# Kernel tuning notes

Hardware: AMD Instinct MI355X
Metric: run time of the kernel (lower is better)

The kernel has to match this reference:

```python
import jax, jax.numpy as jnp
import numpy as np

B, T, C, H = 1, 4096, 512, 8
HS = C // H  # head size = 64
ROPE_BASE = 10000.0


def setup_inputs() -> dict:
    key = jax.random.key(0)
    k1, k2, k3 = jax.random.split(key, 3)
    x = jax.random.normal(k1, (B, T, C), dtype=jnp.float32)
    W_attn = jax.random.normal(k2, (3 * C, C), dtype=jnp.float32) * 0.02
    W_proj = jax.random.normal(k3, (C, C), dtype=jnp.float32) * 0.02
    # RoPE cache: (T, HS//2, 2) = (cos, sin) per position/frequency
    pos = jnp.arange(T, dtype=jnp.float32)
    inv_freq = 1.0 / (ROPE_BASE ** (jnp.arange(0, HS, 2, dtype=jnp.float32) / HS))
    ang = pos[:, None] * inv_freq[None, :]  # (T, HS//2)
    rope = jnp.stack([jnp.cos(ang), jnp.sin(ang)], axis=-1)
    # causal mask (1,1,T,T), True = attend
    mask = jnp.tril(jnp.ones((T, T), dtype=bool))[None, None]
    return {"x": x, "rope": rope, "mask": mask, "W_attn": W_attn, "W_proj": W_proj}


def apply_rope(x, rope):
    # x: (B, T, H, hs); rope: (>=T, hs//2, 2)
    b, t, h, d = x.shape
    xs = x.reshape(b, t, h, d // 2, 2)
    rc = rope[:t].reshape(1, t, 1, d // 2, 2)
    real = xs[..., 0] * rc[..., 0] - xs[..., 1] * rc[..., 1]
    imag = xs[..., 1] * rc[..., 0] + xs[..., 0] * rc[..., 1]
    return jnp.stack([real, imag], axis=-1).reshape(b, t, h, d)


def reference(x, rope, mask, W_attn, W_proj):
    b, t, c = x.shape
    qkv = x @ W_attn.T  # (B,T,3C)
    q, k, v = jnp.split(qkv, 3, axis=2)
    q = q.reshape(b, t, H, HS)
    k = k.reshape(b, t, H, HS)
    v = v.reshape(b, t, H, HS)
    q = apply_rope(q, rope)
    k = apply_rope(k, rope)
    # (B,H,T,hs)
    q = q.transpose(0, 2, 1, 3)
    k = k.transpose(0, 2, 1, 3)
    v = v.transpose(0, 2, 1, 3)
    scores = jnp.einsum('bhqd,bhkd->bhqk', q, k) * (1.0 / np.sqrt(HS).astype(np.float32))
    scores = jnp.where(mask, scores, -jnp.inf)
    att = jax.nn.softmax(scores, axis=-1)
    y = jnp.einsum('bhqk,bhkd->bhqd', att, v)
    y = y.transpose(0, 2, 1, 3).reshape(b, t, c)
    return y @ W_proj.T
```

## Files before the change

kernel.cpp:

```cpp
#include <hip/hip_runtime.h>

#define T_ 4096
#define C_ 512
#define H_ 8
#define HS_ 64

typedef __attribute__((ext_vector_type(8))) short s16x8;
typedef __attribute__((ext_vector_type(4))) float f32x4;
typedef unsigned int u32;

__device__ __forceinline__ float bf2f(short u) {
    union { float f; unsigned int i; } v;
    v.i = ((unsigned int)(unsigned short)u) << 16;
    return v.f;
}
__device__ __forceinline__ short f2bf(float f) {
    union { float f; unsigned int i; } v;
    v.f = f;
    unsigned int r = (v.i + 0x7FFFu + ((v.i >> 16) & 1u)) >> 16;
    return (short)r;
}

__device__ __forceinline__ void gload_lds16(const short* g, short* l) {
    __builtin_amdgcn_global_load_lds((const __attribute__((address_space(1))) u32*)g,
                                     (__attribute__((address_space(3))) u32*)l,
                                     16, 0, 0);
}

__global__ void cvt3_kernel(const float* __restrict__ x, const float* __restrict__ wa,
                            const float* __restrict__ wp,
                            short* __restrict__ xb, short* __restrict__ wab,
                            short* __restrict__ wpb) {
    int b = blockIdx.x, tid = threadIdx.x;
    const float* src; short* dst; int i;
    if (b < 2048)      { src = x;  dst = xb;  i = b * 256 + tid; }
    else if (b < 2816) { src = wa; dst = wab; i = (b - 2048) * 256 + tid; }
    else               { src = wp; dst = wpb; i = (b - 2816) * 256 + tid; }
    float4 v = ((const float4*)src)[i];
    short4 o;
    o.x = f2bf(v.x); o.y = f2bf(v.y); o.z = f2bf(v.z); o.w = f2bf(v.w);
    ((short4*)dst)[i] = o;
}

template <int BM, int BN, int OUT_BF16>
__global__ __launch_bounds__(256) void gemm_bt(const short* __restrict__ A,
                                               const short* __restrict__ B,
                                               void* __restrict__ Cv,
                                               int M, int N, int K) {
    __shared__ __align__(16) short As[BM][64];
    __shared__ __align__(16) short Bs[BN][64];
    constexpr int WM = BM / 2, WN = BN / 2;
    constexpr int MR = WM / 16, NR = WN / 16;
    int bn = blockIdx.x, bm = blockIdx.y;
    int tid = threadIdx.x;
    int lane = tid & 63, w = tid >> 6;
    int wr = w >> 1, wc = w & 1;
    int lr = lane & 15, lg = lane >> 4;

    f32x4 acc[MR][NR];
#pragma unroll
    for (int m = 0; m < MR; ++m)
#pragma unroll
        for (int n = 0; n < NR; ++n) acc[m][n] = f32x4{0.f, 0.f, 0.f, 0.f};

    const short* Ab = A + (size_t)bm * BM * K;
    const short* Bb = B + (size_t)bn * BN * K;

    for (int k0 = 0; k0 < K; k0 += 64) {
#pragma unroll
        for (int i = 0; i < BM / 32; ++i) {
            int c = i * 256 + tid;
            int row = c >> 3, cb = (c & 7) ^ (row & 7);
            gload_lds16(Ab + (size_t)row * K + k0 + cb * 8, &As[0][0] + c * 8);
        }
#pragma unroll
        for (int i = 0; i < BN / 32; ++i) {
            int c = i * 256 + tid;
            int row = c >> 3, cb = (c & 7) ^ (row & 7);
            gload_lds16(Bb + (size_t)row * K + k0 + cb * 8, &Bs[0][0] + c * 8);
        }
        __syncthreads();
#pragma unroll
        for (int kk = 0; kk < 2; ++kk) {
            s16x8 af[MR], bf[NR];
#pragma unroll
            for (int m = 0; m < MR; ++m) {
                int row = wr * WM + m * 16 + lr;
                af[m] = *(const s16x8*)&As[row][(((kk * 4 + lg) ^ (row & 7)) << 3)];
            }
#pragma unroll
            for (int n = 0; n < NR; ++n) {
                int row = wc * WN + n * 16 + lr;
                bf[n] = *(const s16x8*)&Bs[row][(((kk * 4 + lg) ^ (row & 7)) << 3)];
            }
#pragma unroll
            for (int m = 0; m < MR; ++m)
#pragma unroll
                for (int n = 0; n < NR; ++n)
                    acc[m][n] = __builtin_amdgcn_mfma_f32_16x16x32_bf16(af[m], bf[n], acc[m][n], 0, 0, 0);
        }
        __syncthreads();
    }

#pragma unroll
    for (int m = 0; m < MR; ++m) {
        int row = bm * BM + wr * WM + m * 16 + lg * 4;
#pragma unroll
        for (int n = 0; n < NR; ++n) {
            int col = bn * BN + wc * WN + n * 16 + lr;
#pragma unroll
            for (int i = 0; i < 4; ++i) {
                size_t idx = (size_t)(row + i) * N + col;
                if (OUT_BF16) ((short*)Cv)[idx] = f2bf(acc[m][n][i]);
                else          ((float*)Cv)[idx] = acc[m][n][i];
            }
        }
    }
}

__global__ __launch_bounds__(256) void prep_kernel(const short* __restrict__ qkv,
                                                   const float* __restrict__ rope,
                                                   short* __restrict__ q,
                                                   short* __restrict__ k,
                                                   short* __restrict__ vt) {
    __shared__ short tile[64][72];
    int bt = blockIdx.x, h = blockIdx.y;
    int tid = threadIdx.x;
    const float QS = 0.18033688011112042f;

#pragma unroll
    for (int r = 0; r < 2; ++r) {
        int idx = r * 256 + tid;
        int tt = idx >> 3, c8 = idx & 7;
        int t = bt * 64 + tt;
        const short* row = qkv + (size_t)t * (3 * C_) + h * 64 + c8 * 8;
        s16x8 qv = *(const s16x8*)row;
        s16x8 kv = *(const s16x8*)(row + C_);
        float4 rc0 = *(const float4*)(rope + t * 64 + c8 * 8);
        float4 rc1 = *(const float4*)(rope + t * 64 + c8 * 8 + 4);
        float cs[4] = {rc0.x, rc0.z, rc1.x, rc1.z};
        float sn[4] = {rc0.y, rc0.w, rc1.y, rc1.w};
        s16x8 qo, ko;
#pragma unroll
        for (int p = 0; p < 4; ++p) {
            float qe = bf2f(qv[2 * p]), qd = bf2f(qv[2 * p + 1]);
            float ke = bf2f(kv[2 * p]), kd = bf2f(kv[2 * p + 1]);
            qo[2 * p]     = f2bf((qe * cs[p] - qd * sn[p]) * QS);
            qo[2 * p + 1] = f2bf((qd * cs[p] + qe * sn[p]) * QS);
            ko[2 * p]     = f2bf(ke * cs[p] - kd * sn[p]);
            ko[2 * p + 1] = f2bf(kd * cs[p] + ke * sn[p]);
        }
        size_t o = ((size_t)h * T_ + t) * HS_ + c8 * 8;
        *(s16x8*)(q + o) = qo;
        *(s16x8*)(k + o) = ko;
    }

#pragma unroll
    for (int it = 0; it < 16; ++it) {
        int idx = it * 256 + tid;
        int dd = idx & 63, tt = idx >> 6;
        tile[tt][dd] = qkv[(size_t)(bt * 64 + tt) * (3 * C_) + 2 * C_ + h * 64 + dd];
    }
    __syncthreads();
#pragma unroll
    for (int it = 0; it < 16; ++it) {
        int idx = it * 256 + tid;
        int tt = idx & 63, dd = idx >> 6;
        vt[((size_t)h * HS_ + dd) * T_ + bt * 64 + tt] = tile[tt][dd];
    }
}

__global__ __launch_bounds__(256) void attn_kernel(const short* __restrict__ q,
                                                   const short* __restrict__ k,
                                                   const short* __restrict__ vt,
                                                   short* __restrict__ ypart,
                                                   float* __restrict__ lpart) {
    __shared__ __align__(16) short Ks[2][64][64];
    __shared__ __align__(16) short Vs[2][64][64];
    __shared__ __align__(16) short P[4][2][16][64];
    int bx = blockIdx.x;
    int h = bx & 7;
    int rest = bx >> 3;
    int qb = 31 - (rest >> 3);
    int cc = rest & 7;
    int tmax = 2 * qb + 1;
    int t0 = cc * 8;
    if (t0 > tmax) return;
    int t1 = min(t0 + 8, tmax + 1);
    int tid = threadIdx.x;
    int w = tid >> 6, lane = tid & 63;
    int lr = lane & 15, lg = lane >> 4, x7 = lane & 7;
    int qrow0 = qb * 128 + w * 32;
    const float MC = 12.0f;

    const short* qp = q + ((size_t)h * T_ + qrow0 + lr) * HS_ + lg * 8;
    s16x8 aq0 = *(const s16x8*)qp;
    s16x8 aq1 = *(const s16x8*)(qp + 32);
    s16x8 aq2 = *(const s16x8*)(qp + 16 * HS_);
    s16x8 aq3 = *(const s16x8*)(qp + 16 * HS_ + 32);

    s16x8 bones;
#pragma unroll
    for (int j = 0; j < 8; ++j) bones[j] = (short)0x3F80;

    f32x4 yA[4], yB[4];
#pragma unroll
    for (int n = 0; n < 4; ++n) { yA[n] = f32x4{0.f,0.f,0.f,0.f}; yB[n] = f32x4{0.f,0.f,0.f,0.f}; }
    f32x4 lAa = f32x4{0.f,0.f,0.f,0.f}, lBa = f32x4{0.f,0.f,0.f,0.f};

    const short* kH = k + (size_t)h * T_ * HS_;
    const short* vH = vt + (size_t)h * HS_ * T_;

    auto stage = [&](short* Kb, short* Vb, int t) {
#pragma unroll
        for (int r = 0; r < 2; ++r) {
            int c = r * 256 + tid;
            int row = c >> 3;
            int cb = (c & 7) ^ (row & 7);
            gload_lds16(kH + (size_t)(t * 64 + row) * HS_ + cb * 8, Kb + c * 8);
            gload_lds16(vH + (size_t)row * T_ + t * 64 + cb * 8, Vb + c * 8);
        }
    };

    short* PA = &P[w][0][0][0];
    short* PB = &P[w][1][0][0];

    auto body = [&](int t, const short* Kb, const short* Vb) {
        f32x4 sA[4], sB[4];
#pragma unroll
        for (int c4 = 0; c4 < 4; ++c4) {
            int krow = c4 * 16 + lr;
            const short* kp = Kb + krow * 64;
            s16x8 k0 = *(const s16x8*)(kp + ((lg ^ x7) << 3));
            s16x8 k1 = *(const s16x8*)(kp + (((lg + 4) ^ x7) << 3));
            f32x4 s = f32x4{0.f,0.f,0.f,0.f};
            s = __builtin_amdgcn_mfma_f32_16x16x32_bf16(aq0, k0, s, 0, 0, 0);
            sA[c4] = __builtin_amdgcn_mfma_f32_16x16x32_bf16(aq1, k1, s, 0, 0, 0);
            f32x4 s2 = f32x4{0.f,0.f,0.f,0.f};
            s2 = __builtin_amdgcn_mfma_f32_16x16x32_bf16(aq2, k0, s2, 0, 0, 0);
            sB[c4] = __builtin_amdgcn_mfma_f32_16x16x32_bf16(aq3, k1, s2, 0, 0, 0);
        }
        if (t * 64 + 63 > qrow0) {
#pragma unroll
            for (int c4 = 0; c4 < 4; ++c4) {
                int kcol = t * 64 + c4 * 16 + lr;
#pragma unroll
                for (int i = 0; i < 4; ++i)
                    if (kcol > qrow0 + lg * 4 + i) sA[c4][i] = -1e30f;
            }
        }
        if (t * 64 + 63 > qrow0 + 16) {
#pragma unroll
            for (int c4 = 0; c4 < 4; ++c4) {
                int kcol = t * 64 + c4 * 16 + lr;
#pragma unroll
                for (int i = 0; i < 4; ++i)
                    if (kcol > qrow0 + 16 + lg * 4 + i) sB[c4][i] = -1e30f;
            }
        }
#pragma unroll
        for (int c4 = 0; c4 < 4; ++c4)
#pragma unroll
            for (int i = 0; i < 4; ++i) {
                int row = lg * 4 + i;
                int off = row * 64 + (((c4 * 2 + (lr >> 3)) ^ (row & 7)) << 3) + (lr & 7);
                PA[off] = f2bf(exp2f(sA[c4][i] - MC));
                PB[off] = f2bf(exp2f(sB[c4][i] - MC));
            }
        s16x8 apA0 = *(const s16x8*)&PA[lr * 64 + ((lg ^ x7) << 3)];
        s16x8 apA1 = *(const s16x8*)&PA[lr * 64 + (((lg + 4) ^ x7) << 3)];
        s16x8 apB0 = *(const s16x8*)&PB[lr * 64 + ((lg ^ x7) << 3)];
        s16x8 apB1 = *(const s16x8*)&PB[lr * 64 + (((lg + 4) ^ x7) << 3)];

        lAa = __builtin_amdgcn_mfma_f32_16x16x32_bf16(apA0, bones, lAa, 0, 0, 0);
        lAa = __builtin_amdgcn_mfma_f32_16x16x32_bf16(apA1, bones, lAa, 0, 0, 0);
        lBa = __builtin_amdgcn_mfma_f32_16x16x32_bf16(apB0, bones, lBa, 0, 0, 0);
        lBa = __builtin_amdgcn_mfma_f32_16x16x32_bf16(apB1, bones, lBa, 0, 0, 0);

#pragma unroll
        for (int n = 0; n < 4; ++n) {
            int vrow = n * 16 + lr;
            const short* vrp = Vb + vrow * 64;
            s16x8 v0 = *(const s16x8*)(vrp + ((lg ^ x7) << 3));
            s16x8 v1 = *(const s16x8*)(vrp + (((lg + 4) ^ x7) << 3));
            yA[n] = __builtin_amdgcn_mfma_f32_16x16x32_bf16(apA0, v0, yA[n], 0, 0, 0);
            yA[n] = __builtin_amdgcn_mfma_f32_16x16x32_bf16(apA1, v1, yA[n], 0, 0, 0);
            yB[n] = __builtin_amdgcn_mfma_f32_16x16x32_bf16(apB0, v0, yB[n], 0, 0, 0);
            yB[n] = __builtin_amdgcn_mfma_f32_16x16x32_bf16(apB1, v1, yB[n], 0, 0, 0);
        }
    };

    stage(&Ks[0][0][0], &Vs[0][0][0], t0);
    __syncthreads();
    int t = t0;
    for (;;) {
        bool m1 = (t + 1 < t1);
        if (m1) stage(&Ks[1][0][0], &Vs[1][0][0], t + 1);
        body(t, &Ks[0][0][0], &Vs[0][0][0]);
        __syncthreads();
        ++t;
        if (!m1) break;
        bool m2 = (t + 1 < t1);
        if (m2) stage(&Ks[0][0][0], &Vs[0][0][0], t + 1);
        body(t, &Ks[1][0][0], &Vs[1][0][0]);
        __syncthreads();
        ++t;
        if (!m2) break;
    }

    short* yp = ypart + (((size_t)cc * H_ + h) * T_ + qrow0) * HS_;
#pragma unroll
    for (int n = 0; n < 4; ++n)
#pragma unroll
        for (int i = 0; i < 4; ++i) {
            yp[(size_t)(lg * 4 + i) * HS_ + n * 16 + lr]      = f2bf(yA[n][i]);
            yp[(size_t)(16 + lg * 4 + i) * HS_ + n * 16 + lr] = f2bf(yB[n][i]);
        }
    if (lr == 0) {
#pragma unroll
        for (int i = 0; i < 4; ++i) {
            size_t r = ((size_t)cc * H_ + h) * T_ + qrow0;
            lpart[r + lg * 4 + i]      = lAa[i];
            lpart[r + 16 + lg * 4 + i] = lBa[i];
        }
    }
}

__global__ void combine_kernel(const short* __restrict__ ypart,
                               const float* __restrict__ lpart,
                               short* __restrict__ y) {
    int g = blockIdx.x * 256 + threadIdx.x;
    int c8 = (g & 7) * 8;
    int row = (g >> 3) & 4095;
    int h = g >> 15;
    int nc = (row >> 9) + 1;
    float L = 0.f;
    float acc[8] = {0.f, 0.f, 0.f, 0.f, 0.f, 0.f, 0.f, 0.f};
    for (int c = 0; c < nc; ++c) {
        size_t base = ((size_t)c * H_ + h) * T_ + row;
        L += lpart[base];
        s16x8 yv = *(const s16x8*)(ypart + base * HS_ + c8);
#pragma unroll
        for (int j = 0; j < 8; ++j) acc[j] += bf2f(yv[j]);
    }
    float inv = 1.f / L;
    s16x8 o;
#pragma unroll
    for (int j = 0; j < 8; ++j) o[j] = f2bf(acc[j] * inv);
    *(s16x8*)(y + (size_t)row * C_ + h * 64 + c8) = o;
}

extern "C" void kernel_launch(void* const* d_in, const int* in_sizes, int n_in,
                              void* d_out, int out_size, void* d_ws, size_t ws_size,
                              hipStream_t stream) {
    const float* x    = (const float*)d_in[0];
    const float* rope = (const float*)d_in[1];
    const float* Wa   = (const float*)d_in[3];
    const float* Wp   = (const float*)d_in[4];
    float* out = (float*)d_out;

    short* ws   = (short*)d_ws;
    short* xb   = ws;
    short* wab  = xb + 2097152;
    short* wpb  = wab + 786432;
    short* qkvb = wpb + 262144;
    short* qws  = qkvb + 6291456;
    short* kws  = qws + 2097152;
    short* vtws = kws + 2097152;
    short* yws  = vtws + 2097152;
    short* ypart = yws + 2097152;
    float* lpart = (float*)(ypart + 16777216);

    cvt3_kernel<<<3072, 256, 0, stream>>>(x, Wa, Wp, xb, wab, wpb);

    gemm_bt<128, 64, 1><<<dim3(24, 32), 256, 0, stream>>>(xb, wab, qkvb, 4096, 1536, 512);

    prep_kernel<<<dim3(64, 8), 256, 0, stream>>>(qkvb, rope, qws, kws, vtws);

    attn_kernel<<<2048, 256, 0, stream>>>(qws, kws, vtws, ypart, lpart);
    combine_kernel<<<1024, 256, 0, stream>>>(ypart, lpart, yws);

    gemm_bt<64, 64, 0><<<dim3(8, 64), 256, 0, stream>>>(yws, wpb, out, 4096, 512, 512);
}
```

Before: 190.4 us.

## Balance split-KV attention work per query block and retune GEMM tiles

Each query block now gets a number of KV chunks that grows with its causal length, and the KV tiles are spread evenly across those chunks. This replaces the fixed 8-tile chunks that launched many empty blocks and left the rest unevenly loaded; the combine kernel's chunk count is updated to match. The attention body also reuses a single per-warp P buffer for the two 16-row halves and loads the V fragments once, which halves P's LDS footprint but serialises the two halves. Both projection GEMMs switch to larger tiles with fewer blocks, which cuts block overhead but may reduce occupancy.

```diff
diff --git a/kernel.cpp b/kernel.cpp
--- a/kernel.cpp
+++ b/kernel.cpp
@@ -177,16 +177,22 @@
                                                    float* __restrict__ lpart) {
     __shared__ __align__(16) short Ks[2][64][64];
     __shared__ __align__(16) short Vs[2][64][64];
-    __shared__ __align__(16) short P[4][2][16][64];
+    __shared__ __align__(16) short P[4][16][64];
     int bx = blockIdx.x;
     int h = bx & 7;
-    int rest = bx >> 3;
-    int qb = 31 - (rest >> 3);
-    int cc = rest & 7;
-    int tmax = 2 * qb + 1;
-    int t0 = cc * 8;
-    if (t0 > tmax) return;
-    int t1 = min(t0 + 8, tmax + 1);
+    int u = bx >> 3;
+    int qb = 0, j = u;
+    for (int qq = 31; qq >= 0; --qq) {
+        int ncq = (qq + 4) >> 2;
+        if (j < ncq) { qb = qq; break; }
+        j -= ncq;
+    }
+    int ncq = (qb + 4) >> 2;
+    int tiles = 2 * qb + 2;
+    int bas = tiles / ncq, rr = tiles % ncq;
+    int t0 = j * bas + (j < rr ? j : rr);
+    int t1 = t0 + bas + (j < rr ? 1 : 0);
+
     int tid = threadIdx.x;
     int w = tid >> 6, lane = tid & 63;
     int lr = lane & 15, lg = lane >> 4, x7 = lane & 7;
@@ -201,7 +207,7 @@
 
     s16x8 bones;
 #pragma unroll
-    for (int j = 0; j < 8; ++j) bones[j] = (short)0x3F80;
+    for (int jj = 0; jj < 8; ++jj) bones[jj] = (short)0x3F80;
 
     f32x4 yA[4], yB[4];
 #pragma unroll
@@ -222,8 +228,7 @@
         }
     };
 
-    short* PA = &P[w][0][0][0];
-    short* PB = &P[w][1][0][0];
+    short* Pw = &P[w][0][0];
 
     auto body = [&](int t, const short* Kb, const short* Vb) {
         f32x4 sA[4], sB[4];
@@ -258,35 +263,47 @@
                     if (kcol > qrow0 + 16 + lg * 4 + i) sB[c4][i] = -1e30f;
             }
         }
+        s16x8 vf[8];
+#pragma unroll
+        for (int n = 0; n < 4; ++n) {
+            int vrow = n * 16 + lr;
+            const short* vrp = Vb + vrow * 64;
+            vf[2 * n]     = *(const s16x8*)(vrp + ((lg ^ (vrow & 7)) << 3));
+            vf[2 * n + 1] = *(const s16x8*)(vrp + (((lg + 4) ^ (vrow & 7)) << 3));
+        }
 #pragma unroll
         for (int c4 = 0; c4 < 4; ++c4)
 #pragma unroll
             for (int i = 0; i < 4; ++i) {
                 int row = lg * 4 + i;
                 int off = row * 64 + (((c4 * 2 + (lr >> 3)) ^ (row & 7)) << 3) + (lr & 7);
-                PA[off] = f2bf(exp2f(sA[c4][i] - MC));
-                PB[off] = f2bf(exp2f(sB[c4][i] - MC));
-            }
-        s16x8 apA0 = *(const s16x8*)&PA[lr * 64 + ((lg ^ x7) << 3)];
-        s16x8 apA1 = *(const s16x8*)&PA[lr * 64 + (((lg + 4) ^ x7) << 3)];
-        s16x8 apB0 = *(const s16x8*)&PB[lr * 64 + ((lg ^ x7) << 3)];
-        s16x8 apB1 = *(const s16x8*)&PB[lr * 64 + (((lg + 4) ^ x7) << 3)];
-
-        lAa = __builtin_amdgcn_mfma_f32_16x16x32_bf16(apA0, bones, lAa, 0, 0, 0);
-        lAa = __builtin_amdgcn_mfma_f32_16x16x32_bf16(apA1, bones, lAa, 0, 0, 0);
-        lBa = __builtin_amdgcn_mfma_f32_16x16x32_bf16(apB0, bones, lBa, 0, 0, 0);
-        lBa = __builtin_amdgcn_mfma_f32_16x16x32_bf16(apB1, bones, lBa, 0, 0, 0);
-
+                Pw[off] = f2bf(exp2f(sA[c4][i] - MC));
+            }
+        s16x8 ap0 = *(const s16x8*)&Pw[lr * 64 + ((lg ^ x7) << 3)];
+        s16x8 ap1 = *(const s16x8*)&Pw[lr * 64 + (((lg + 4) ^ x7) << 3)];
+        lAa = __builtin_amdgcn_mfma_f32_16x16x32_bf16(ap0, bones, lAa, 0, 0, 0);
+        lAa = __builtin_amdgcn_mfma_f32_16x16x32_bf16(ap1, bones, lAa, 0, 0, 0);
 #pragma unroll
         for (int n = 0; n < 4; ++n) {
-            int vrow = n * 16 + lr;
-            const short* vrp = Vb + vrow * 64;
-            s16x8 v0 = *(const s16x8*)(vrp + ((lg ^ x7) << 3));
-            s16x8 v1 = *(const s16x8*)(vrp + (((lg + 4) ^ x7) << 3));
-            yA[n] = __builtin_amdgcn_mfma_f32_16x16x32_bf16(apA0, v0, yA[n], 0, 0, 0);
-            yA[n] = __builtin_amdgcn_mfma_f32_16x16x32_bf16(apA1, v1, yA[n], 0, 0, 0);
-            yB[n] = __builtin_amdgcn_mfma_f32_16x16x32_bf16(apB0, v0, yB[n], 0, 0, 0);
-            yB[n] = __builtin_amdgcn_mfma_f32_16x16x32_bf16(apB1, v1, yB[n], 0, 0, 0);
+            yA[n] = __builtin_amdgcn_mfma_f32_16x16x32_bf16(ap0, vf[2 * n], yA[n], 0, 0, 0);
+            yA[n] = __builtin_amdgcn_mfma_f32_16x16x32_bf16(ap1, vf[2 * n + 1], yA[n], 0, 0, 0);
+        }
+#pragma unroll
+        for (int c4 = 0; c4 < 4; ++c4)
+#pragma unroll
+            for (int i = 0; i < 4; ++i) {
+                int row = lg * 4 + i;
+                int off = row * 64 + (((c4 * 2 + (lr >> 3)) ^ (row & 7)) << 3) + (lr & 7);
+                Pw[off] = f2bf(exp2f(sB[c4][i] - MC));
+            }
+        s16x8 bp0 = *(const s16x8*)&Pw[lr * 64 + ((lg ^ x7) << 3)];
+        s16x8 bp1 = *(const s16x8*)&Pw[lr * 64 + (((lg + 4) ^ x7) << 3)];
+        lBa = __builtin_amdgcn_mfma_f32_16x16x32_bf16(bp0, bones, lBa, 0, 0, 0);
+        lBa = __builtin_amdgcn_mfma_f32_16x16x32_bf16(bp1, bones, lBa, 0, 0, 0);
+#pragma unroll
+        for (int n = 0; n < 4; ++n) {
+            yB[n] = __builtin_amdgcn_mfma_f32_16x16x32_bf16(bp0, vf[2 * n], yB[n], 0, 0, 0);
+            yB[n] = __builtin_amdgcn_mfma_f32_16x16x32_bf16(bp1, vf[2 * n + 1], yB[n], 0, 0, 0);
         }
     };
 
@@ -308,7 +325,7 @@
         if (!m2) break;
     }
 
-    short* yp = ypart + (((size_t)cc * H_ + h) * T_ + qrow0) * HS_;
+    short* yp = ypart + (((size_t)j * H_ + h) * T_ + qrow0) * HS_;
 #pragma unroll
     for (int n = 0; n < 4; ++n)
 #pragma unroll
@@ -319,7 +336,7 @@
     if (lr == 0) {
 #pragma unroll
         for (int i = 0; i < 4; ++i) {
-            size_t r = ((size_t)cc * H_ + h) * T_ + qrow0;
+            size_t r = ((size_t)j * H_ + h) * T_ + qrow0;
             lpart[r + lg * 4 + i]      = lAa[i];
             lpart[r + 16 + lg * 4 + i] = lBa[i];
         }
@@ -333,7 +350,7 @@
     int c8 = (g & 7) * 8;
     int row = (g >> 3) & 4095;
     int h = g >> 15;
-    int nc = (row >> 9) + 1;
+    int nc = ((row >> 7) + 4) >> 2;
     float L = 0.f;
     float acc[8] = {0.f, 0.f, 0.f, 0.f, 0.f, 0.f, 0.f, 0.f};
     for (int c = 0; c < nc; ++c) {
@@ -341,12 +358,12 @@
         L += lpart[base];
         s16x8 yv = *(const s16x8*)(ypart + base * HS_ + c8);
 #pragma unroll
-        for (int j = 0; j < 8; ++j) acc[j] += bf2f(yv[j]);
+        for (int jj = 0; jj < 8; ++jj) acc[jj] += bf2f(yv[jj]);
     }
     float inv = 1.f / L;
     s16x8 o;
 #pragma unroll
-    for (int j = 0; j < 8; ++j) o[j] = f2bf(acc[j] * inv);
+    for (int jj = 0; jj < 8; ++jj) o[jj] = f2bf(acc[jj] * inv);
     *(s16x8*)(y + (size_t)row * C_ + h * 64 + c8) = o;
 }
 
@@ -373,12 +390,12 @@
 
     cvt3_kernel<<<3072, 256, 0, stream>>>(x, Wa, Wp, xb, wab, wpb);
 
-    gemm_bt<128, 64, 1><<<dim3(24, 32), 256, 0, stream>>>(xb, wab, qkvb, 4096, 1536, 512);
+    gemm_bt<128, 128, 1><<<dim3(12, 32), 256, 0, stream>>>(xb, wab, qkvb, 4096, 1536, 512);
 
     prep_kernel<<<dim3(64, 8), 256, 0, stream>>>(qkvb, rope, qws, kws, vtws);
 
-    attn_kernel<<<2048, 256, 0, stream>>>(qws, kws, vtws, ypart, lpart);
+    attn_kernel<<<1152, 256, 0, stream>>>(qws, kws, vtws, ypart, lpart);
     combine_kernel<<<1024, 256, 0, stream>>>(ypart, lpart, yws);
 
-    gemm_bt<64, 64, 0><<<dim3(8, 64), 256, 0, stream>>>(yws, wpb, out, 4096, 512, 512);
-}
+    gemm_bt<128, 64, 0><<<dim3(8, 32), 256, 0, stream>>>(yws, wpb, out, 4096, 512, 512);
+}
```

New measurement: 195.2 us. +2.5%, slower.
